# Kernel optimization log

Measured on AMD Instinct MI355X. Metric: run time of the kernel, lower is better.

The kernel has to match this reference:

```python
import jax, jax.numpy as jnp
import numpy as np

NBITS = 4
GROUP_SIZE = 128


def setup_inputs() -> dict:
    key = jax.random.key(0)
    k1, k2, k3, k4, k5 = jax.random.split(key, 5)
    B, S, K, N = 2, 2048, 4096, 4096
    G = K // GROUP_SIZE  # 32 groups along K
    x = jax.random.normal(k1, (B, S, K), dtype=jnp.float16)
    # unpacked uint4 weights stored in int32 carrier, values in [0, 2^nbits)
    W_q = jax.random.randint(k2, (N, K), 0, 2 ** NBITS, dtype=jnp.int32)
    scale = (jax.random.uniform(k3, (N, G), dtype=jnp.float32) * 0.01 + 0.001).astype(jnp.float16)
    zero = (jax.random.uniform(k4, (N, G), dtype=jnp.float32) * (2 ** NBITS)).astype(jnp.float16)
    bias = jax.random.normal(k5, (N,), dtype=jnp.float16)
    return {"x": x, "W_q": W_q, "scale": scale, "zero": zero, "bias": bias}


def _dequant(W_q, scale, zero):
    # W_q: [N, K] int, scale/zero: [N, K//group_size] fp16
    # zeros_mode='original': W = (W_q - zero) * scale, per group along K
    N, K = W_q.shape
    G = K // GROUP_SIZE
    Wg = W_q.reshape(N, G, GROUP_SIZE).astype(jnp.float16)
    Wd = (Wg - zero[:, :, None]) * scale[:, :, None]
    return Wd.reshape(N, K)


def reference(x, W_q, scale, zero, bias):
    # out = x @ W_deq^T + bias   (layout 'nt': W is [N, K])
    W = _dequant(W_q, scale, zero)            # [N, K] fp16
    out = jnp.einsum('bsk,nk->bsn', x, W)     # [B, S, N] fp16 accum per module config
    return out + bias
```

## Files before the change

kernel.cpp:

```cpp
#include <hip/hip_runtime.h>
#include <hip/hip_bf16.h>


typedef __bf16 bf16x8 __attribute__((ext_vector_type(8)));
typedef float f32x4 __attribute__((ext_vector_type(4)));

#define BM 128
#define BN 128
#define BK 64

static __device__ __forceinline__ int pack_bf16x2(float a, float b) {
    __hip_bfloat162 p = __float22bfloat162_rn(make_float2(a, b));
    int r;
    __builtin_memcpy(&r, &p, 4);
    return r;
}

__global__ __launch_bounds__(256) void convert_x_kernel(
    const float* __restrict__ X, unsigned short* __restrict__ Ad)
{
    const long long idx = (long long)blockIdx.x * blockDim.x + threadIdx.x;
    const long long f = idx * 8;
    const float4 a0 = *(const float4*)(X + f);
    const float4 a1 = *(const float4*)(X + f + 4);
    int4 d;
    d.x = pack_bf16x2(a0.x, a0.y);
    d.y = pack_bf16x2(a0.z, a0.w);
    d.z = pack_bf16x2(a1.x, a1.y);
    d.w = pack_bf16x2(a1.z, a1.w);
    *(int4*)(Ad + f) = d;
}

__global__ __launch_bounds__(256) void dequant_kernel(
    const int*   __restrict__ Wq,
    const float* __restrict__ scale,
    const float* __restrict__ zero,
    unsigned short* __restrict__ Wd,
    int K, int G, int GROUP)
{
    const long long idx = (long long)blockIdx.x * blockDim.x + threadIdx.x;
    const long long f = idx * 8;
    const int n = (int)(f / K);
    const int k = (int)(f - (long long)n * K);
    const int g = k / GROUP;
    const float s  = scale[(long long)n * G + g];
    const float z  = zero [(long long)n * G + g];
    const float mz = -z * s;

    const int4 q0 = *(const int4*)(Wq + f);
    const int4 q1 = *(const int4*)(Wq + f + 4);
    int4 d;
    d.x = pack_bf16x2((float)q0.x * s + mz, (float)q0.y * s + mz);
    d.y = pack_bf16x2((float)q0.z * s + mz, (float)q0.w * s + mz);
    d.z = pack_bf16x2((float)q1.x * s + mz, (float)q1.y * s + mz);
    d.w = pack_bf16x2((float)q1.z * s + mz, (float)q1.w * s + mz);
    *(int4*)(Wd + f) = d;
}

__global__ __launch_bounds__(256, 2) void gemm_bf16_nt(
    const unsigned short* __restrict__ A,
    const unsigned short* __restrict__ Bw,
    const float* __restrict__ bias,
    float*       __restrict__ C,
    int M, int N, int K)
{
    __shared__ unsigned short ldsA[BM * BK];
    __shared__ unsigned short ldsB[BN * BK];

    const int tid   = threadIdx.x;
    const int lane  = tid & 63;
    const int wave  = tid >> 6;
    const int waveM = wave >> 1;
    const int waveN = wave & 1;

    const int blockN0 = blockIdx.x * BN;
    const int blockM0 = blockIdx.y * BM;

    const long long aBase = (long long)blockM0 * K;
    const long long bBase = (long long)blockN0 * K;

    const int rowInChunk = lane >> 3;
    const int col8       = (lane & 7) * 8;

    f32x4 acc[4][4];
#pragma unroll
    for (int i = 0; i < 4; ++i)
#pragma unroll
        for (int j = 0; j < 4; ++j)
            acc[i][j] = (f32x4){0.f, 0.f, 0.f, 0.f};

    const int row16 = lane & 15;
    const int quad  = lane >> 4;

    for (int k0 = 0; k0 < K; k0 += BK) {
        __syncthreads();
#pragma unroll
        for (int c = 0; c < 4; ++c) {
            const int chunk = (wave << 2) | c;
            const int row   = (chunk << 3) | rowInChunk;
            const unsigned short* gA = A  + aBase + (long long)row * K + k0 + col8;
            const unsigned short* gB = Bw + bBase + (long long)row * K + k0 + col8;
            __builtin_amdgcn_global_load_lds(
                (const __attribute__((address_space(1))) unsigned int*)gA,
                (__attribute__((address_space(3))) unsigned int*)&ldsA[chunk * 512],
                16, 0, 0);
            __builtin_amdgcn_global_load_lds(
                (const __attribute__((address_space(1))) unsigned int*)gB,
                (__attribute__((address_space(3))) unsigned int*)&ldsB[chunk * 512],
                16, 0, 0);
        }
        __syncthreads();

#pragma unroll
        for (int kk = 0; kk < 2; ++kk) {
            const int kOff = kk * 32 + quad * 8;
            bf16x8 av[4], bv[4];
#pragma unroll
            for (int i = 0; i < 4; ++i)
                av[i] = *(const bf16x8*)&ldsA[(waveM * 64 + i * 16 + row16) * BK + kOff];
#pragma unroll
            for (int j = 0; j < 4; ++j)
                bv[j] = *(const bf16x8*)&ldsB[(waveN * 64 + j * 16 + row16) * BK + kOff];
#pragma unroll
            for (int i = 0; i < 4; ++i)
#pragma unroll
                for (int j = 0; j < 4; ++j)
                    acc[i][j] = __builtin_amdgcn_mfma_f32_16x16x32_bf16(
                        av[i], bv[j], acc[i][j], 0, 0, 0);
        }
    }

    const int colBase = blockN0 + waveN * 64;
    const int rowBase = blockM0 + waveM * 64;
    float biasf[4];
#pragma unroll
    for (int j = 0; j < 4; ++j)
        biasf[j] = bias[colBase + j * 16 + row16];

#pragma unroll
    for (int i = 0; i < 4; ++i) {
        const int row0 = rowBase + i * 16 + quad * 4;
#pragma unroll
        for (int j = 0; j < 4; ++j) {
            const int col = colBase + j * 16 + row16;
#pragma unroll
            for (int r = 0; r < 4; ++r) {
                C[(long long)(row0 + r) * N + col] = acc[i][j][r] + biasf[j];
            }
        }
    }
}

__global__ __launch_bounds__(256) void hqq_gemm_fused_f32(
    const float* __restrict__ A,
    const int*   __restrict__ Wq,
    const float* __restrict__ scale,
    const float* __restrict__ zero,
    const float* __restrict__ bias,
    float*       __restrict__ C,
    int M, int N, int K, int G, int GROUP)
{
    __shared__ unsigned short ldsA[BM * BK];
    __shared__ unsigned short ldsB[BN * BK];

    const int tid   = threadIdx.x;
    const int lane  = tid & 63;
    const int wave  = tid >> 6;
    const int waveM = wave >> 1;
    const int waveN = wave & 1;

    const int blockN0 = blockIdx.x * BN;
    const int blockM0 = blockIdx.y * BM;

    const int row16 = lane & 15;
    const int quad  = lane >> 4;

    f32x4 acc[4][4];
#pragma unroll
    for (int i = 0; i < 4; ++i)
#pragma unroll
        for (int j = 0; j < 4; ++j)
            acc[i][j] = (f32x4){0.f, 0.f, 0.f, 0.f};

    for (int k0 = 0; k0 < K; k0 += BK) {
        const int g = k0 / GROUP;
        int4 ra[4], rb[4];
#pragma unroll
        for (int c = 0; c < 4; ++c) {
            const int chunk = c * 256 + tid;
            const int row   = chunk >> 3;
            const int col   = (chunk & 7) * 8;

            const float* ap = A + (long long)(blockM0 + row) * K + k0 + col;
            const float4 a0 = *(const float4*)(ap);
            const float4 a1 = *(const float4*)(ap + 4);
            int4 da;
            da.x = pack_bf16x2(a0.x, a0.y);
            da.y = pack_bf16x2(a0.z, a0.w);
            da.z = pack_bf16x2(a1.x, a1.y);
            da.w = pack_bf16x2(a1.z, a1.w);
            ra[c] = da;

            const int n = blockN0 + row;
            const float s  = scale[(long long)n * G + g];
            const float z  = zero [(long long)n * G + g];
            const float mz = -z * s;
            const long long wb = (long long)n * K + k0 + col;
            const int4 q0 = *(const int4*)(Wq + wb);
            const int4 q1 = *(const int4*)(Wq + wb + 4);
            int4 db;
            db.x = pack_bf16x2((float)q0.x * s + mz, (float)q0.y * s + mz);
            db.y = pack_bf16x2((float)q0.z * s + mz, (float)q0.w * s + mz);
            db.z = pack_bf16x2((float)q1.x * s + mz, (float)q1.y * s + mz);
            db.w = pack_bf16x2((float)q1.z * s + mz, (float)q1.w * s + mz);
            rb[c] = db;
        }

        __syncthreads();
#pragma unroll
        for (int c = 0; c < 4; ++c) {
            const int chunk = c * 256 + tid;
            *(int4*)&ldsA[chunk * 8] = ra[c];
            *(int4*)&ldsB[chunk * 8] = rb[c];
        }
        __syncthreads();

#pragma unroll
        for (int kk = 0; kk < 2; ++kk) {
            const int kOff = kk * 32 + quad * 8;
            bf16x8 av[4], bv[4];
#pragma unroll
            for (int i = 0; i < 4; ++i)
                av[i] = *(const bf16x8*)&ldsA[(waveM * 64 + i * 16 + row16) * BK + kOff];
#pragma unroll
            for (int j = 0; j < 4; ++j)
                bv[j] = *(const bf16x8*)&ldsB[(waveN * 64 + j * 16 + row16) * BK + kOff];
#pragma unroll
            for (int i = 0; i < 4; ++i)
#pragma unroll
                for (int j = 0; j < 4; ++j)
                    acc[i][j] = __builtin_amdgcn_mfma_f32_16x16x32_bf16(
                        av[i], bv[j], acc[i][j], 0, 0, 0);
        }
    }

    const int colBase = blockN0 + waveN * 64;
    const int rowBase = blockM0 + waveM * 64;
    float biasf[4];
#pragma unroll
    for (int j = 0; j < 4; ++j)
        biasf[j] = bias[colBase + j * 16 + row16];

#pragma unroll
    for (int i = 0; i < 4; ++i) {
        const int row0 = rowBase + i * 16 + quad * 4;
#pragma unroll
        for (int j = 0; j < 4; ++j) {
            const int col = colBase + j * 16 + row16;
#pragma unroll
            for (int r = 0; r < 4; ++r) {
                C[(long long)(row0 + r) * N + col] = acc[i][j][r] + biasf[j];
            }
        }
    }
}

extern "C" void kernel_launch(void* const* d_in, const int* in_sizes, int n_in,
                              void* d_out, int out_size, void* d_ws, size_t ws_size,
                              hipStream_t stream) {
    (void)n_in; (void)out_size;

    const float* x     = (const float*)d_in[0];
    const int*   Wq    = (const int*)d_in[1];
    const float* scale = (const float*)d_in[2];
    const float* zero  = (const float*)d_in[3];
    const float* bias  = (const float*)d_in[4];
    float*       out   = (float*)d_out;

    const int N     = in_sizes[4];
    const int G     = in_sizes[2] / N;
    const int K     = in_sizes[1] / N;
    const int M     = in_sizes[0] / K;
    const int GROUP = K / G;

    const size_t needWs = (size_t)N * K * 2 + (size_t)M * K * 2;

    if (ws_size >= needWs) {
        unsigned short* Wd = (unsigned short*)d_ws;
        unsigned short* Ad = (unsigned short*)((char*)d_ws + (size_t)N * K * 2);

        const long long totalW = (long long)N * K / 8;
        dequant_kernel<<<(int)(totalW / 256), 256, 0, stream>>>(Wq, scale, zero, Wd,
                                                                K, G, GROUP);
        const long long totalA = (long long)M * K / 8;
        convert_x_kernel<<<(int)(totalA / 256), 256, 0, stream>>>(x, Ad);

        dim3 grid(N / BN, M / BM);
        gemm_bf16_nt<<<grid, 256, 0, stream>>>(Ad, Wd, bias, out, M, N, K);
    } else {
        dim3 grid(N / BN, M / BM);
        hqq_gemm_fused_f32<<<grid, 256, 0, stream>>>(x, Wq, scale, zero, bias, out,
                                                     M, N, K, G, GROUP);
    }
}
```

Before: 344.7 us.

## Merge prepass kernels, switch GEMM to 32x32x16 MFMA with XOR-swizzled LDS

Folds the weight dequant and activation bf16 conversion into a single launch, so one kernel launch and its tail are removed. The GEMM inner loop moves from 16x16x32 to 32x32x16 bf16 MFMA tiles, which cuts the number of LDS fragment loads per MFMA. The LDS layout gets an XOR swizzle on the 16-byte column slot to avoid bank conflicts on the fragment reads. The epilogue is rewritten to the 32x32 accumulator layout, and the prepass now uses 32-bit unsigned index math.

Result: faster. 322.1 us (-6.5%).

```diff
diff --git a/kernel.cpp b/kernel.cpp
--- a/kernel.cpp
+++ b/kernel.cpp
@@ -4,6 +4,7 @@
 
 typedef __bf16 bf16x8 __attribute__((ext_vector_type(8)));
 typedef float f32x4 __attribute__((ext_vector_type(4)));
+typedef float f32x16 __attribute__((ext_vector_type(16)));
 
 #define BM 128
 #define BN 128
@@ -16,45 +17,45 @@
     return r;
 }
 
-__global__ __launch_bounds__(256) void convert_x_kernel(
-    const float* __restrict__ X, unsigned short* __restrict__ Ad)
-{
-    const long long idx = (long long)blockIdx.x * blockDim.x + threadIdx.x;
-    const long long f = idx * 8;
-    const float4 a0 = *(const float4*)(X + f);
-    const float4 a1 = *(const float4*)(X + f + 4);
-    int4 d;
-    d.x = pack_bf16x2(a0.x, a0.y);
-    d.y = pack_bf16x2(a0.z, a0.w);
-    d.z = pack_bf16x2(a1.x, a1.y);
-    d.w = pack_bf16x2(a1.z, a1.w);
-    *(int4*)(Ad + f) = d;
-}
-
-__global__ __launch_bounds__(256) void dequant_kernel(
+__global__ __launch_bounds__(256) void prepass_kernel(
+    const float* __restrict__ X,
     const int*   __restrict__ Wq,
     const float* __restrict__ scale,
     const float* __restrict__ zero,
+    unsigned short* __restrict__ Ad,
     unsigned short* __restrict__ Wd,
-    int K, int G, int GROUP)
+    int K, int G, int GROUP, int nWBlocks)
 {
-    const long long idx = (long long)blockIdx.x * blockDim.x + threadIdx.x;
-    const long long f = idx * 8;
-    const int n = (int)(f / K);
-    const int k = (int)(f - (long long)n * K);
-    const int g = k / GROUP;
-    const float s  = scale[(long long)n * G + g];
-    const float z  = zero [(long long)n * G + g];
-    const float mz = -z * s;
-
-    const int4 q0 = *(const int4*)(Wq + f);
-    const int4 q1 = *(const int4*)(Wq + f + 4);
-    int4 d;
-    d.x = pack_bf16x2((float)q0.x * s + mz, (float)q0.y * s + mz);
-    d.y = pack_bf16x2((float)q0.z * s + mz, (float)q0.w * s + mz);
-    d.z = pack_bf16x2((float)q1.x * s + mz, (float)q1.y * s + mz);
-    d.w = pack_bf16x2((float)q1.z * s + mz, (float)q1.w * s + mz);
-    *(int4*)(Wd + f) = d;
+    const int b = blockIdx.x;
+    if (b < nWBlocks) {
+        const unsigned int idx = (unsigned int)b * 256u + threadIdx.x;
+        const unsigned int f = idx * 8u;
+        const unsigned int n = f / (unsigned int)K;
+        const unsigned int k = f - n * (unsigned int)K;
+        const unsigned int g = k / (unsigned int)GROUP;
+        const float s  = scale[(size_t)n * G + g];
+        const float z  = zero [(size_t)n * G + g];
+        const float mz = -z * s;
+        const int4 q0 = *(const int4*)(Wq + f);
+        const int4 q1 = *(const int4*)(Wq + f + 4);
+        int4 d;
+        d.x = pack_bf16x2((float)q0.x * s + mz, (float)q0.y * s + mz);
+        d.y = pack_bf16x2((float)q0.z * s + mz, (float)q0.w * s + mz);
+        d.z = pack_bf16x2((float)q1.x * s + mz, (float)q1.y * s + mz);
+        d.w = pack_bf16x2((float)q1.z * s + mz, (float)q1.w * s + mz);
+        *(int4*)(Wd + f) = d;
+    } else {
+        const unsigned int idx = (unsigned int)(b - nWBlocks) * 256u + threadIdx.x;
+        const unsigned int f = idx * 8u;
+        const float4 a0 = *(const float4*)(X + f);
+        const float4 a1 = *(const float4*)(X + f + 4);
+        int4 d;
+        d.x = pack_bf16x2(a0.x, a0.y);
+        d.y = pack_bf16x2(a0.z, a0.w);
+        d.z = pack_bf16x2(a1.x, a1.y);
+        d.w = pack_bf16x2(a1.z, a1.w);
+        *(int4*)(Ad + f) = d;
+    }
 }
 
 __global__ __launch_bounds__(256, 2) void gemm_bf16_nt(
@@ -80,17 +81,18 @@
     const long long bBase = (long long)blockN0 * K;
 
     const int rowInChunk = lane >> 3;
-    const int col8       = (lane & 7) * 8;
-
-    f32x4 acc[4][4];
-#pragma unroll
-    for (int i = 0; i < 4; ++i)
-#pragma unroll
-        for (int j = 0; j < 4; ++j)
-            acc[i][j] = (f32x4){0.f, 0.f, 0.f, 0.f};
-
-    const int row16 = lane & 15;
-    const int quad  = lane >> 4;
+    const int col8       = ((lane & 7) ^ rowInChunk) * 8;
+
+    f32x16 acc[2][2];
+#pragma unroll
+    for (int i = 0; i < 2; ++i)
+#pragma unroll
+        for (int j = 0; j < 2; ++j)
+            acc[i][j] = (f32x16)(0.f);
+
+    const int lrow  = lane & 31;
+    const int khalf = lane >> 5;
+    const int sw    = lane & 7;
 
     for (int k0 = 0; k0 < K; k0 += BK) {
         __syncthreads();
@@ -112,40 +114,40 @@
         __syncthreads();
 
 #pragma unroll
-        for (int kk = 0; kk < 2; ++kk) {
-            const int kOff = kk * 32 + quad * 8;
-            bf16x8 av[4], bv[4];
-#pragma unroll
-            for (int i = 0; i < 4; ++i)
-                av[i] = *(const bf16x8*)&ldsA[(waveM * 64 + i * 16 + row16) * BK + kOff];
-#pragma unroll
-            for (int j = 0; j < 4; ++j)
-                bv[j] = *(const bf16x8*)&ldsB[(waveN * 64 + j * 16 + row16) * BK + kOff];
-#pragma unroll
-            for (int i = 0; i < 4; ++i)
-#pragma unroll
-                for (int j = 0; j < 4; ++j)
-                    acc[i][j] = __builtin_amdgcn_mfma_f32_16x16x32_bf16(
-                        av[i], bv[j], acc[i][j], 0, 0, 0);
+        for (int ks = 0; ks < 4; ++ks) {
+            const int slot = ((ks << 1) | khalf) ^ sw;
+            bf16x8 av[2], bv[2];
+#pragma unroll
+            for (int mi = 0; mi < 2; ++mi)
+                av[mi] = *(const bf16x8*)&ldsA[(waveM * 64 + mi * 32 + lrow) * BK + slot * 8];
+#pragma unroll
+            for (int nj = 0; nj < 2; ++nj)
+                bv[nj] = *(const bf16x8*)&ldsB[(waveN * 64 + nj * 32 + lrow) * BK + slot * 8];
+#pragma unroll
+            for (int mi = 0; mi < 2; ++mi)
+#pragma unroll
+                for (int nj = 0; nj < 2; ++nj)
+                    acc[mi][nj] = __builtin_amdgcn_mfma_f32_32x32x16_bf16(
+                        av[mi], bv[nj], acc[mi][nj], 0, 0, 0);
         }
     }
 
     const int colBase = blockN0 + waveN * 64;
     const int rowBase = blockM0 + waveM * 64;
-    float biasf[4];
-#pragma unroll
-    for (int j = 0; j < 4; ++j)
-        biasf[j] = bias[colBase + j * 16 + row16];
-
-#pragma unroll
-    for (int i = 0; i < 4; ++i) {
-        const int row0 = rowBase + i * 16 + quad * 4;
-#pragma unroll
-        for (int j = 0; j < 4; ++j) {
-            const int col = colBase + j * 16 + row16;
-#pragma unroll
-            for (int r = 0; r < 4; ++r) {
-                C[(long long)(row0 + r) * N + col] = acc[i][j][r] + biasf[j];
+    float biasf[2];
+#pragma unroll
+    for (int nj = 0; nj < 2; ++nj)
+        biasf[nj] = bias[colBase + nj * 32 + lrow];
+
+#pragma unroll
+    for (int mi = 0; mi < 2; ++mi) {
+#pragma unroll
+        for (int nj = 0; nj < 2; ++nj) {
+            const int col = colBase + nj * 32 + lrow;
+#pragma unroll
+            for (int r = 0; r < 16; ++r) {
+                const int row = rowBase + mi * 32 + (r & 3) + 8 * (r >> 2) + 4 * khalf;
+                C[(long long)row * N + col] = acc[mi][nj][r] + biasf[nj];
             }
         }
     }
@@ -289,11 +291,10 @@
         unsigned short* Wd = (unsigned short*)d_ws;
         unsigned short* Ad = (unsigned short*)((char*)d_ws + (size_t)N * K * 2);
 
-        const long long totalW = (long long)N * K / 8;
-        dequant_kernel<<<(int)(totalW / 256), 256, 0, stream>>>(Wq, scale, zero, Wd,
-                                                                K, G, GROUP);
-        const long long totalA = (long long)M * K / 8;
-        convert_x_kernel<<<(int)(totalA / 256), 256, 0, stream>>>(x, Ad);
+        const int nWBlocks = (int)((long long)N * K / 8 / 256);
+        const int nABlocks = (int)((long long)M * K / 8 / 256);
+        prepass_kernel<<<nWBlocks + nABlocks, 256, 0, stream>>>(
+            x, Wq, scale, zero, Ad, Wd, K, G, GROUP, nWBlocks);
 
         dim3 grid(N / BN, M / BM);
         gemm_bf16_nt<<<grid, 256, 0, stream>>>(Ad, Wd, bias, out, M, N, K);
```
